# Optimization experiments

Hardware: AMD Instinct MI355X
Metric: run time of the kernel (lower is better)

## Reference

```python
import jax, jax.numpy as jnp
import numpy as np

N = 100000          # nodes
E = 1600000         # edges
F = 128             # input features
H = 128             # hidden_channels
G = 64              # graphs in batch


def setup_inputs() -> dict:
    key = jax.random.key(0)
    ks = jax.random.split(key, 16)
    x = jax.random.normal(ks[0], (N, F), dtype=jnp.float32)
    edge_index = jax.random.randint(ks[1], (2, E), 0, N, dtype=jnp.int32)
    batch = jnp.sort(jax.random.randint(ks[2], (N,), 0, G, dtype=jnp.int32))

    def glorot(k, fan_in, fan_out):
        s = jnp.sqrt(6.0 / (fan_in + fan_out)).astype(jnp.float32)
        return jax.random.uniform(k, (fan_in, fan_out), jnp.float32, -s, s)

    return {
        "x": x, "edge_index": edge_index, "batch": batch,
        "W1": glorot(ks[3], F, H),       "b1": jnp.zeros((H,), jnp.float32),
        "W2": glorot(ks[4], H, H),       "b2": jnp.zeros((H,), jnp.float32),
        "W3": glorot(ks[5], H, 2 * H),   "b3": jnp.zeros((2 * H,), jnp.float32),
        "W4": glorot(ks[6], 2 * H, H),   "b4": jnp.zeros((H,), jnp.float32),
        "Wl": glorot(ks[7], F, H),       "bl": jnp.zeros((H,), jnp.float32),
    }


def _gcn_conv(x, W, b, src, dst, deg_inv_sqrt):
    # PyG GCNConv: add self-loops, symmetric normalization D^-1/2 (A+I) D^-1/2
    h = x @ W                                  # [N, out]
    norm = deg_inv_sqrt[src] * deg_inv_sqrt[dst]      # [E]
    msg = h[src] * norm[:, None]               # gather + scale, [E, out]
    agg = jax.ops.segment_sum(msg, dst, num_segments=N)
    agg = agg + h * (deg_inv_sqrt * deg_inv_sqrt)[:, None]  # self-loop term (norm = 1/deg)
    return agg + b


def reference(x, edge_index, batch, W1, b1, W2, b2, W3, b3, W4, b4, Wl, bl):
    src, dst = edge_index[0], edge_index[1]
    # degree (incl. self-loop) from dst, as in PyG gcn_norm
    deg = jax.ops.segment_sum(jnp.ones((E,), jnp.float32), dst, num_segments=N) + 1.0
    deg_inv_sqrt = jax.lax.rsqrt(deg)

    identity = x
    x = jax.nn.relu(_gcn_conv(x, W1, b1, src, dst, deg_inv_sqrt))
    x = jax.nn.relu(_gcn_conv(x, W2, b2, src, dst, deg_inv_sqrt))
    x = jax.nn.relu(_gcn_conv(x, W3, b3, src, dst, deg_inv_sqrt))
    x = _gcn_conv(x, W4, b4, src, dst, deg_inv_sqrt)
    x = x + (identity @ Wl + bl)

    # global_mean_pool over graph ids
    sums = jax.ops.segment_sum(x, batch, num_segments=G)
    cnts = jax.ops.segment_sum(jnp.ones((N,), jnp.float32), batch, num_segments=G)
    return sums / jnp.maximum(cnts, 1.0)[:, None]
```

## Files before the change

kernel.cpp:

```cpp
#include <hip/hip_runtime.h>

#define NN 100000
#define EE 1600000
#define GG 64

typedef __attribute__((ext_vector_type(8))) short short8v;
typedef __attribute__((ext_vector_type(4))) float f32x4;

__device__ __forceinline__ unsigned short f2bf(float f) {
    unsigned u = __float_as_uint(f);
    u = (u + 0x7FFFu + ((u >> 16) & 1)) >> 16;
    return (unsigned short)u;
}
__device__ __forceinline__ float bf2f(unsigned short s) {
    return __uint_as_float((unsigned)s << 16);
}

__global__ __launch_bounds__(256) void count_kernel(const int* __restrict__ dst,
                                                    int* __restrict__ cnt) {
    int e = blockIdx.x * 256 + threadIdx.x;
    if (e < EE) atomicAdd(&cnt[dst[e]], 1);
}

__global__ __launch_bounds__(256) void dis_kernel(const int* __restrict__ cnt,
                                                  float* __restrict__ dis) {
    int i = blockIdx.x * 256 + threadIdx.x;
    if (i < NN) dis[i] = rsqrtf((float)cnt[i] + 1.0f);
}

#define SCAN_EPB 1024
__global__ __launch_bounds__(256) void scan_block_kernel(const int* __restrict__ in,
                                                         int* __restrict__ out,
                                                         int* __restrict__ bsums) {
    __shared__ int sd[256];
    int t = threadIdx.x;
    int base = blockIdx.x * SCAN_EPB + t * 4;
    int v[4];
#pragma unroll
    for (int j = 0; j < 4; ++j) v[j] = (base + j < NN) ? in[base + j] : 0;
    int s = v[0] + v[1] + v[2] + v[3];
    sd[t] = s;
    __syncthreads();
    for (int off = 1; off < 256; off <<= 1) {
        int add = (t >= off) ? sd[t - off] : 0;
        __syncthreads();
        sd[t] += add;
        __syncthreads();
    }
    int ex = sd[t] - s;
    int run = ex;
#pragma unroll
    for (int j = 0; j < 4; ++j) {
        if (base + j < NN) out[base + j] = run;
        run += v[j];
    }
    if (t == 255) bsums[blockIdx.x] = sd[255];
}

__global__ void scan_sums_kernel(int* __restrict__ bsums, int nb) {
    if (threadIdx.x == 0 && blockIdx.x == 0) {
        int run = 0;
        for (int i = 0; i < nb; ++i) {
            int v = bsums[i];
            bsums[i] = run;
            run += v;
        }
    }
}

__global__ __launch_bounds__(256) void scan_add_kernel(int* __restrict__ rs,
                                                       const int* __restrict__ bsums,
                                                       int* __restrict__ cursor) {
    int i = blockIdx.x * 256 + threadIdx.x;
    if (i < NN) {
        int v = rs[i] + bsums[i >> 10];
        rs[i] = v;
        cursor[i] = v;
    }
    if (i == 0) rs[NN] = EE;
}

__global__ __launch_bounds__(256) void scatter_kernel(const int* __restrict__ src,
                                                      const int* __restrict__ dst,
                                                      const float* __restrict__ dis,
                                                      int* __restrict__ cursor,
                                                      int2* __restrict__ csr) {
    int e = blockIdx.x * 256 + threadIdx.x;
    if (e < EE) {
        int d = dst[e], s = src[e];
        int p = atomicAdd(&cursor[d], 1);
        csr[p] = make_int2(s, __float_as_int(dis[s]));
    }
}

__global__ __launch_bounds__(256) void cvt_kernel(const float* __restrict__ x,
                                                  unsigned short* __restrict__ xb) {
    size_t i = ((size_t)blockIdx.x * 256 + threadIdx.x) * 8;
    float4 a = *(const float4*)(x + i);
    float4 b = *(const float4*)(x + i + 4);
    short8v v;
    v[0] = (short)f2bf(a.x); v[1] = (short)f2bf(a.y);
    v[2] = (short)f2bf(a.z); v[3] = (short)f2bf(a.w);
    v[4] = (short)f2bf(b.x); v[5] = (short)f2bf(b.y);
    v[6] = (short)f2bf(b.z); v[7] = (short)f2bf(b.w);
    *(short8v*)(xb + i) = v;
}

template <int K, int M>
__global__ __launch_bounds__(64) void packw_kernel(const float* __restrict__ W,
                                                   unsigned short* __restrict__ Wp) {
    const int NKS = K / 32;
    int ct = blockIdx.x / NKS, ks = blockIdx.x % NKS;
    int lane = threadIdx.x;
    int col = ct * 16 + (lane & 15);
    int kb = ks * 32 + (lane >> 4) * 8;
    unsigned short* o = Wp + ((size_t)(ct * NKS + ks) * 64 + lane) * 16;
#pragma unroll
    for (int i = 0; i < 8; ++i) {
        float f = W[(size_t)(kb + i) * M + col];
        unsigned short h = f2bf(f);
        unsigned short l = f2bf(f - bf2f(h));
        o[i] = h;
        o[8 + i] = l;
    }
}

template <int K, int M, bool ASPLIT, bool RELU, bool BIAS, bool ACCUM>
__global__ __launch_bounds__(256) void gemm_kernel(const void* __restrict__ Ain,
                                                   const unsigned short* __restrict__ Wp,
                                                   const float* __restrict__ bias,
                                                   void* __restrict__ out) {
    const int NKS = K / 32;
    int tid = threadIdx.x;
    int wave = tid >> 6, lane = tid & 63;
    int r0 = blockIdx.x * 64 + wave * 16;
    int ra = r0 + (lane & 15);
    if (ra > NN - 1) ra = NN - 1;

    short8v ah[NKS];
    short8v al[ASPLIT ? NKS : 1];
    if (ASPLIT) {
        const float* A = (const float*)Ain;
#pragma unroll
        for (int ks = 0; ks < NKS; ++ks) {
            const float* p = A + (size_t)ra * K + ks * 32 + (lane >> 4) * 8;
            float4 v0 = *(const float4*)p;
            float4 v1 = *(const float4*)(p + 4);
            float f[8] = {v0.x, v0.y, v0.z, v0.w, v1.x, v1.y, v1.z, v1.w};
#pragma unroll
            for (int i = 0; i < 8; ++i) {
                unsigned short h = f2bf(f[i]);
                ah[ks][i] = (short)h;
                al[ks][i] = (short)f2bf(f[i] - bf2f(h));
            }
        }
    } else {
        const unsigned short* A = (const unsigned short*)Ain;
#pragma unroll
        for (int ks = 0; ks < NKS; ++ks)
            ah[ks] = *(const short8v*)(A + (size_t)ra * K + ks * 32 + (lane >> 4) * 8);
    }

#pragma unroll
    for (int ct = 0; ct < 8; ++ct) {
        int ctg = blockIdx.y * 8 + ct;
        int col = ctg * 16 + (lane & 15);
        float b = BIAS ? bias[col] : 0.f;
        f32x4 acc;
        acc[0] = b; acc[1] = b; acc[2] = b; acc[3] = b;
#pragma unroll
        for (int ks = 0; ks < NKS; ++ks) {
            const short8v* p = (const short8v*)Wp + ((size_t)(ctg * NKS + ks) * 64 + lane) * 2;
            short8v bh = p[0], bl = p[1];
            acc = __builtin_amdgcn_mfma_f32_16x16x32_bf16(ah[ks], bh, acc, 0, 0, 0);
            acc = __builtin_amdgcn_mfma_f32_16x16x32_bf16(ah[ks], bl, acc, 0, 0, 0);
            if (ASPLIT)
                acc = __builtin_amdgcn_mfma_f32_16x16x32_bf16(al[ks], bh, acc, 0, 0, 0);
        }
#pragma unroll
        for (int i = 0; i < 4; ++i) {
            int row = r0 + (lane >> 4) * 4 + i;
            if (row >= NN) continue;
            float v = acc[i];
            if (RELU) v = fmaxf(v, 0.f);
            if (ACCUM) {
                float* Y = (float*)out;
                Y[(size_t)row * M + col] += v;
            } else {
                unsigned short* O = (unsigned short*)out;
                O[(size_t)row * M + col] = f2bf(v);
            }
        }
    }
}

template <int OUTMODE>
__global__ __launch_bounds__(256) void aggb_kernel(const unsigned short* __restrict__ h,
                                                   const float* __restrict__ dis,
                                                   const int2* __restrict__ csr,
                                                   const int* __restrict__ rs,
                                                   const float* __restrict__ bias,
                                                   void* __restrict__ out) {
    int node = blockIdx.x * 4 + (threadIdx.x >> 6);
    int lane = threadIdx.x & 63;
    if (node >= NN) return;
    int c = lane & 15;
    int s = lane >> 4;
    int beg = rs[node], end = rs[node + 1];
    const uint4* hb = (const uint4*)h;
    float acc[8] = {};
    for (int e0 = beg; e0 < end; e0 += 4) {
        int e = e0 + s;
        int ec = e < end ? e : end - 1;
        int2 pr = csr[ec];
        float w = e < end ? __int_as_float(pr.y) : 0.f;
        uint4 v = hb[(size_t)pr.x * 16 + c];
        acc[0] = fmaf(w, __uint_as_float(v.x << 16), acc[0]);
        acc[1] = fmaf(w, __uint_as_float(v.x & 0xFFFF0000u), acc[1]);
        acc[2] = fmaf(w, __uint_as_float(v.y << 16), acc[2]);
        acc[3] = fmaf(w, __uint_as_float(v.y & 0xFFFF0000u), acc[3]);
        acc[4] = fmaf(w, __uint_as_float(v.z << 16), acc[4]);
        acc[5] = fmaf(w, __uint_as_float(v.z & 0xFFFF0000u), acc[5]);
        acc[6] = fmaf(w, __uint_as_float(v.w << 16), acc[6]);
        acc[7] = fmaf(w, __uint_as_float(v.w & 0xFFFF0000u), acc[7]);
    }
#pragma unroll
    for (int i = 0; i < 8; ++i) {
        acc[i] += __shfl_xor(acc[i], 16, 64);
        acc[i] += __shfl_xor(acc[i], 32, 64);
    }
    if (s == 0) {
        float d = dis[node];
        float dd = d * d;
        uint4 us = hb[(size_t)node * 16 + c];
        float sf[8];
        sf[0] = __uint_as_float(us.x << 16); sf[1] = __uint_as_float(us.x & 0xFFFF0000u);
        sf[2] = __uint_as_float(us.y << 16); sf[3] = __uint_as_float(us.y & 0xFFFF0000u);
        sf[4] = __uint_as_float(us.z << 16); sf[5] = __uint_as_float(us.z & 0xFFFF0000u);
        sf[6] = __uint_as_float(us.w << 16); sf[7] = __uint_as_float(us.w & 0xFFFF0000u);
        float r[8];
#pragma unroll
        for (int i = 0; i < 8; ++i) r[i] = fmaf(d, acc[i], dd * sf[i]);
        if (OUTMODE == 0) {
            uint4 o;
            o.x = (unsigned)f2bf(r[0]) | ((unsigned)f2bf(r[1]) << 16);
            o.y = (unsigned)f2bf(r[2]) | ((unsigned)f2bf(r[3]) << 16);
            o.z = (unsigned)f2bf(r[4]) | ((unsigned)f2bf(r[5]) << 16);
            o.w = (unsigned)f2bf(r[6]) | ((unsigned)f2bf(r[7]) << 16);
            ((uint4*)out)[(size_t)node * 16 + c] = o;
        } else {
#pragma unroll
            for (int i = 0; i < 8; ++i) r[i] += bias[c * 8 + i];
            float4 o0 = make_float4(r[0], r[1], r[2], r[3]);
            float4 o1 = make_float4(r[4], r[5], r[6], r[7]);
            float* O = (float*)out + (size_t)node * 128 + c * 8;
            *(float4*)O = o0;
            *(float4*)(O + 4) = o1;
        }
    }
}

__global__ __launch_bounds__(128) void pool_partial_kernel(const float* __restrict__ y,
                                                           const int* __restrict__ batch,
                                                           float* __restrict__ P) {
    int c = threadIdx.x;
    int chunk = (NN + gridDim.x - 1) / gridDim.x;
    int n0 = blockIdx.x * chunk;
    int n1 = n0 + chunk;
    if (n1 > NN) n1 = NN;
    if (n0 >= NN) return;
    int curg = batch[n0];
    float acc = 0.f;
    for (int n = n0; n < n1; ++n) {
        int g = batch[n];
        if (g != curg) {
            atomicAdd(&P[curg * 128 + c], acc);
            acc = 0.f;
            curg = g;
        }
        acc += y[(size_t)n * 128 + c];
    }
    atomicAdd(&P[curg * 128 + c], acc);
}

__global__ __launch_bounds__(128) void pool_final_kernel(const float* __restrict__ P,
                                                         const int* __restrict__ batch,
                                                         float* __restrict__ out) {
    int g = blockIdx.x, c = threadIdx.x;
    int lo = 0, hi = NN;
    while (lo < hi) {
        int m = (lo + hi) >> 1;
        if (batch[m] < g) lo = m + 1;
        else hi = m;
    }
    int start = lo;
    int lo2 = start, hi2 = NN;
    while (lo2 < hi2) {
        int m = (lo2 + hi2) >> 1;
        if (batch[m] < g + 1) lo2 = m + 1;
        else hi2 = m;
    }
    float cntg = (float)(lo2 - start);
    out[g * 128 + c] = P[g * 128 + c] / fmaxf(cntg, 1.f);
}

extern "C" void kernel_launch(void* const* d_in, const int* in_sizes, int n_in,
                              void* d_out, int out_size, void* d_ws, size_t ws_size,
                              hipStream_t stream) {
    const float* x = (const float*)d_in[0];
    const int* ei = (const int*)d_in[1];
    const int* batch = (const int*)d_in[2];
    const float* W1 = (const float*)d_in[3];
    const float* b1 = (const float*)d_in[4];
    const float* W2 = (const float*)d_in[5];
    const float* b2 = (const float*)d_in[6];
    const float* W3 = (const float*)d_in[7];
    const float* b3 = (const float*)d_in[8];
    const float* W4 = (const float*)d_in[9];
    const float* b4 = (const float*)d_in[10];
    const float* Wl = (const float*)d_in[11];
    const float* bl = (const float*)d_in[12];
    float* out = (float*)d_out;

    char* p = (char*)d_ws;
    auto alloc = [&](size_t bytes) {
        void* r = (void*)p;
        p += (bytes + 255) & ~(size_t)255;
        return r;
    };
    int* cnt = (int*)alloc((size_t)NN * 4);
    int* rs = (int*)alloc((size_t)(NN + 1) * 4);
    int* cursor = (int*)alloc((size_t)NN * 4);
    float* dis = (float*)alloc((size_t)NN * 4);
    const int NB = (NN + SCAN_EPB - 1) / SCAN_EPB;
    int* bsums = (int*)alloc((size_t)NB * 4);
    int2* csr = (int2*)alloc((size_t)EE * 8);
    unsigned short* xb = (unsigned short*)alloc((size_t)NN * 128 * 2);
    unsigned short* AG = (unsigned short*)alloc((size_t)NN * 128 * 2);
    unsigned short* GM = (unsigned short*)alloc((size_t)NN * 128 * 2);
    unsigned short* H3 = (unsigned short*)alloc((size_t)NN * 256 * 2);
    float* Y = (float*)alloc((size_t)NN * 128 * 4);
    unsigned short* W1p = (unsigned short*)alloc(8 * 4 * 64 * 16 * 2);
    unsigned short* W2p = (unsigned short*)alloc(8 * 4 * 64 * 16 * 2);
    unsigned short* W3p = (unsigned short*)alloc(16 * 4 * 64 * 16 * 2);
    unsigned short* W4p = (unsigned short*)alloc(8 * 8 * 64 * 16 * 2);
    unsigned short* Wlp = (unsigned short*)alloc(8 * 4 * 64 * 16 * 2);
    float* P = (float*)alloc((size_t)GG * 128 * 4);

    const int* src = ei;
    const int* dst = ei + EE;

    hipMemsetAsync(cnt, 0, (size_t)NN * 4, stream);
    hipMemsetAsync(P, 0, (size_t)GG * 128 * 4, stream);

    count_kernel<<<EE / 256, 256, 0, stream>>>(dst, cnt);
    dis_kernel<<<(NN + 255) / 256, 256, 0, stream>>>(cnt, dis);
    scan_block_kernel<<<NB, 256, 0, stream>>>(cnt, rs, bsums);
    scan_sums_kernel<<<1, 64, 0, stream>>>(bsums, NB);
    scan_add_kernel<<<(NN + 255) / 256, 256, 0, stream>>>(rs, bsums, cursor);
    scatter_kernel<<<EE / 256, 256, 0, stream>>>(src, dst, dis, cursor, csr);

    cvt_kernel<<<(NN * 128) / (256 * 8), 256, 0, stream>>>(x, xb);
    packw_kernel<128, 128><<<8 * 4, 64, 0, stream>>>(W1, W1p);
    packw_kernel<128, 128><<<8 * 4, 64, 0, stream>>>(W2, W2p);
    packw_kernel<128, 256><<<16 * 4, 64, 0, stream>>>(W3, W3p);
    packw_kernel<256, 128><<<8 * 8, 64, 0, stream>>>(W4, W4p);
    packw_kernel<128, 128><<<8 * 4, 64, 0, stream>>>(Wl, Wlp);

    const int AGG_GRID = (NN + 3) / 4;
    const int GX = (NN + 63) / 64;

    aggb_kernel<0><<<AGG_GRID, 256, 0, stream>>>(xb, dis, csr, rs, nullptr, AG);
    gemm_kernel<128, 128, false, true, true, false><<<dim3(GX, 1), 256, 0, stream>>>(AG, W1p, b1, GM);
    aggb_kernel<0><<<AGG_GRID, 256, 0, stream>>>(GM, dis, csr, rs, nullptr, AG);
    gemm_kernel<128, 128, false, true, true, false><<<dim3(GX, 1), 256, 0, stream>>>(AG, W2p, b2, GM);
    aggb_kernel<0><<<AGG_GRID, 256, 0, stream>>>(GM, dis, csr, rs, nullptr, AG);
    gemm_kernel<128, 256, false, true, true, false><<<dim3(GX, 2), 256, 0, stream>>>(AG, W3p, b3, H3);
    gemm_kernel<256, 128, false, false, false, false><<<dim3(GX, 1), 256, 0, stream>>>(H3, W4p, nullptr, AG);
    aggb_kernel<1><<<AGG_GRID, 256, 0, stream>>>(AG, dis, csr, rs, b4, Y);
    gemm_kernel<128, 128, true, false, true, true><<<dim3(GX, 1), 256, 0, stream>>>(x, Wlp, bl, Y);
    pool_partial_kernel<<<512, 128, 0, stream>>>(Y, batch, P);
    pool_final_kernel<<<GG, 128, 0, stream>>>(P, batch, out);
}
```

Before: 820.6 us.

## Bucket edges before CSR scatter, add row tiling to GEMM, unroll aggregation

Edges are first binned into coarse destination buckets of 256 nodes. A per-bucket scatter pass then writes CSR entries, so the cursor atomics and writes stay localized. The GEMM kernel now processes several 16-row tiles per wave, which reuses each loaded weight fragment across more rows. The aggregation loop issues four gathers before doing the FMAs, to raise memory-level parallelism. Buckets have a fixed capacity of 8192 and any overflow is silently clamped, which relies on dst being roughly uniform. The bucket buffer also reuses the Y allocation.

```diff
diff --git a/kernel.cpp b/kernel.cpp
--- a/kernel.cpp
+++ b/kernel.cpp
@@ -3,6 +3,8 @@
 #define NN 100000
 #define EE 1600000
 #define GG 64
+#define NBK 391
+#define BCAP 8192
 
 typedef __attribute__((ext_vector_type(8))) short short8v;
 typedef __attribute__((ext_vector_type(4))) float f32x4;
@@ -16,10 +18,20 @@
     return __uint_as_float((unsigned)s << 16);
 }
 
-__global__ __launch_bounds__(256) void count_kernel(const int* __restrict__ dst,
-                                                    int* __restrict__ cnt) {
+__global__ __launch_bounds__(256) void bucket_kernel(const int* __restrict__ src,
+                                                     const int* __restrict__ dst,
+                                                     int* __restrict__ cnt,
+                                                     int* __restrict__ bcur,
+                                                     int2* __restrict__ bbuf) {
     int e = blockIdx.x * 256 + threadIdx.x;
-    if (e < EE) atomicAdd(&cnt[dst[e]], 1);
+    if (e < EE) {
+        int d = dst[e], s = src[e];
+        atomicAdd(&cnt[d], 1);
+        int b = d >> 8;
+        int p = atomicAdd(&bcur[b], 1);
+        if (p >= BCAP) p = BCAP - 1;
+        bbuf[(size_t)b * BCAP + p] = make_int2(s, d);
+    }
 }
 
 __global__ __launch_bounds__(256) void dis_kernel(const int* __restrict__ cnt,
@@ -80,16 +92,19 @@
     if (i == 0) rs[NN] = EE;
 }
 
-__global__ __launch_bounds__(256) void scatter_kernel(const int* __restrict__ src,
-                                                      const int* __restrict__ dst,
-                                                      const float* __restrict__ dis,
-                                                      int* __restrict__ cursor,
-                                                      int2* __restrict__ csr) {
-    int e = blockIdx.x * 256 + threadIdx.x;
-    if (e < EE) {
-        int d = dst[e], s = src[e];
-        int p = atomicAdd(&cursor[d], 1);
-        csr[p] = make_int2(s, __float_as_int(dis[s]));
+__global__ __launch_bounds__(256) void scatter2_kernel(const int2* __restrict__ bbuf,
+                                                       const int* __restrict__ bcur,
+                                                       const float* __restrict__ dis,
+                                                       int* __restrict__ cursor,
+                                                       int2* __restrict__ csr) {
+    int b = blockIdx.x;
+    int n = bcur[b];
+    if (n > BCAP) n = BCAP;
+    const int2* bb = bbuf + (size_t)b * BCAP;
+    for (int i = threadIdx.x; i < n; i += 256) {
+        int2 e = bb[i];
+        int p = atomicAdd(&cursor[e.y], 1);
+        csr[p] = make_int2(e.x, __float_as_int(dis[e.x]));
     }
 }
 
@@ -125,7 +140,7 @@
     }
 }
 
-template <int K, int M, bool ASPLIT, bool RELU, bool BIAS, bool ACCUM>
+template <int K, int M, int RT, bool ASPLIT, bool RELU, bool BIAS, bool ACCUM>
 __global__ __launch_bounds__(256) void gemm_kernel(const void* __restrict__ Ain,
                                                    const unsigned short* __restrict__ Wp,
                                                    const float* __restrict__ bias,
@@ -133,64 +148,73 @@
     const int NKS = K / 32;
     int tid = threadIdx.x;
     int wave = tid >> 6, lane = tid & 63;
-    int r0 = blockIdx.x * 64 + wave * 16;
-    int ra = r0 + (lane & 15);
-    if (ra > NN - 1) ra = NN - 1;
-
-    short8v ah[NKS];
-    short8v al[ASPLIT ? NKS : 1];
-    if (ASPLIT) {
-        const float* A = (const float*)Ain;
-#pragma unroll
-        for (int ks = 0; ks < NKS; ++ks) {
-            const float* p = A + (size_t)ra * K + ks * 32 + (lane >> 4) * 8;
-            float4 v0 = *(const float4*)p;
-            float4 v1 = *(const float4*)(p + 4);
-            float f[8] = {v0.x, v0.y, v0.z, v0.w, v1.x, v1.y, v1.z, v1.w};
-#pragma unroll
-            for (int i = 0; i < 8; ++i) {
-                unsigned short h = f2bf(f[i]);
-                ah[ks][i] = (short)h;
-                al[ks][i] = (short)f2bf(f[i] - bf2f(h));
+    int r0 = blockIdx.x * (RT * 64) + wave * (RT * 16);
+
+    short8v ah[RT][NKS];
+    short8v al[ASPLIT ? RT : 1][ASPLIT ? NKS : 1];
+#pragma unroll
+    for (int t = 0; t < RT; ++t) {
+        int ra = r0 + t * 16 + (lane & 15);
+        if (ra > NN - 1) ra = NN - 1;
+        if (ASPLIT) {
+            const float* A = (const float*)Ain;
+#pragma unroll
+            for (int ks = 0; ks < NKS; ++ks) {
+                const float* p = A + (size_t)ra * K + ks * 32 + (lane >> 4) * 8;
+                float4 v0 = *(const float4*)p;
+                float4 v1 = *(const float4*)(p + 4);
+                float f[8] = {v0.x, v0.y, v0.z, v0.w, v1.x, v1.y, v1.z, v1.w};
+#pragma unroll
+                for (int i = 0; i < 8; ++i) {
+                    unsigned short h = f2bf(f[i]);
+                    ah[t][ks][i] = (short)h;
+                    al[t][ks][i] = (short)f2bf(f[i] - bf2f(h));
+                }
             }
-        }
-    } else {
-        const unsigned short* A = (const unsigned short*)Ain;
-#pragma unroll
-        for (int ks = 0; ks < NKS; ++ks)
-            ah[ks] = *(const short8v*)(A + (size_t)ra * K + ks * 32 + (lane >> 4) * 8);
+        } else {
+            const unsigned short* A = (const unsigned short*)Ain;
+#pragma unroll
+            for (int ks = 0; ks < NKS; ++ks)
+                ah[t][ks] = *(const short8v*)(A + (size_t)ra * K + ks * 32 + (lane >> 4) * 8);
+        }
     }
 
 #pragma unroll
     for (int ct = 0; ct < 8; ++ct) {
         int ctg = blockIdx.y * 8 + ct;
         int col = ctg * 16 + (lane & 15);
-        float b = BIAS ? bias[col] : 0.f;
-        f32x4 acc;
-        acc[0] = b; acc[1] = b; acc[2] = b; acc[3] = b;
+        float bv = BIAS ? bias[col] : 0.f;
+        f32x4 acc[RT];
+#pragma unroll
+        for (int t = 0; t < RT; ++t) {
+            acc[t][0] = bv; acc[t][1] = bv; acc[t][2] = bv; acc[t][3] = bv;
+        }
 #pragma unroll
         for (int ks = 0; ks < NKS; ++ks) {
-            const short8v* p = (const short8v*)Wp + ((size_t)(ctg * NKS + ks) * 64 + lane) * 2;
-            short8v bh = p[0], bl = p[1];
-            acc = __builtin_amdgcn_mfma_f32_16x16x32_bf16(ah[ks], bh, acc, 0, 0, 0);
-            acc = __builtin_amdgcn_mfma_f32_16x16x32_bf16(ah[ks], bl, acc, 0, 0, 0);
-            if (ASPLIT)
-                acc = __builtin_amdgcn_mfma_f32_16x16x32_bf16(al[ks], bh, acc, 0, 0, 0);
-        }
-#pragma unroll
-        for (int i = 0; i < 4; ++i) {
-            int row = r0 + (lane >> 4) * 4 + i;
-            if (row >= NN) continue;
-            float v = acc[i];
-            if (RELU) v = fmaxf(v, 0.f);
-            if (ACCUM) {
-                float* Y = (float*)out;
-                Y[(size_t)row * M + col] += v;
-            } else {
-                unsigned short* O = (unsigned short*)out;
-                O[(size_t)row * M + col] = f2bf(v);
+            const short8v* pW = (const short8v*)Wp + ((size_t)(ctg * NKS + ks) * 64 + lane) * 2;
+            short8v bh = pW[0], blo = pW[1];
+#pragma unroll
+            for (int t = 0; t < RT; ++t) {
+                acc[t] = __builtin_amdgcn_mfma_f32_16x16x32_bf16(ah[t][ks], bh, acc[t], 0, 0, 0);
+                acc[t] = __builtin_amdgcn_mfma_f32_16x16x32_bf16(ah[t][ks], blo, acc[t], 0, 0, 0);
+                if (ASPLIT)
+                    acc[t] = __builtin_amdgcn_mfma_f32_16x16x32_bf16(al[t][ks], bh, acc[t], 0, 0, 0);
             }
         }
+#pragma unroll
+        for (int t = 0; t < RT; ++t)
+#pragma unroll
+            for (int i = 0; i < 4; ++i) {
+                int row = r0 + t * 16 + (lane >> 4) * 4 + i;
+                if (row >= NN) continue;
+                float v = acc[t][i];
+                if (RELU) v = fmaxf(v, 0.f);
+                if (ACCUM) {
+                    ((float*)out)[(size_t)row * M + col] += v;
+                } else {
+                    ((unsigned short*)out)[(size_t)row * M + col] = f2bf(v);
+                }
+            }
     }
 }
 
@@ -209,20 +233,28 @@
     int beg = rs[node], end = rs[node + 1];
     const uint4* hb = (const uint4*)h;
     float acc[8] = {};
-    for (int e0 = beg; e0 < end; e0 += 4) {
-        int e = e0 + s;
-        int ec = e < end ? e : end - 1;
-        int2 pr = csr[ec];
-        float w = e < end ? __int_as_float(pr.y) : 0.f;
-        uint4 v = hb[(size_t)pr.x * 16 + c];
-        acc[0] = fmaf(w, __uint_as_float(v.x << 16), acc[0]);
-        acc[1] = fmaf(w, __uint_as_float(v.x & 0xFFFF0000u), acc[1]);
-        acc[2] = fmaf(w, __uint_as_float(v.y << 16), acc[2]);
-        acc[3] = fmaf(w, __uint_as_float(v.y & 0xFFFF0000u), acc[3]);
-        acc[4] = fmaf(w, __uint_as_float(v.z << 16), acc[4]);
-        acc[5] = fmaf(w, __uint_as_float(v.z & 0xFFFF0000u), acc[5]);
-        acc[6] = fmaf(w, __uint_as_float(v.w << 16), acc[6]);
-        acc[7] = fmaf(w, __uint_as_float(v.w & 0xFFFF0000u), acc[7]);
+    for (int e0 = beg; e0 < end; e0 += 16) {
+        float w[4];
+        uint4 v[4];
+#pragma unroll
+        for (int j = 0; j < 4; ++j) {
+            int ej = e0 + j * 4 + s;
+            int ec = ej < end ? ej : end - 1;
+            int2 pr = csr[ec];
+            w[j] = ej < end ? __int_as_float(pr.y) : 0.f;
+            v[j] = hb[(size_t)pr.x * 16 + c];
+        }
+#pragma unroll
+        for (int j = 0; j < 4; ++j) {
+            acc[0] = fmaf(w[j], __uint_as_float(v[j].x << 16), acc[0]);
+            acc[1] = fmaf(w[j], __uint_as_float(v[j].x & 0xFFFF0000u), acc[1]);
+            acc[2] = fmaf(w[j], __uint_as_float(v[j].y << 16), acc[2]);
+            acc[3] = fmaf(w[j], __uint_as_float(v[j].y & 0xFFFF0000u), acc[3]);
+            acc[4] = fmaf(w[j], __uint_as_float(v[j].z << 16), acc[4]);
+            acc[5] = fmaf(w[j], __uint_as_float(v[j].z & 0xFFFF0000u), acc[5]);
+            acc[6] = fmaf(w[j], __uint_as_float(v[j].w << 16), acc[6]);
+            acc[7] = fmaf(w[j], __uint_as_float(v[j].w & 0xFFFF0000u), acc[7]);
+        }
     }
 #pragma unroll
     for (int i = 0; i < 8; ++i) {
@@ -334,6 +366,7 @@
     float* dis = (float*)alloc((size_t)NN * 4);
     const int NB = (NN + SCAN_EPB - 1) / SCAN_EPB;
     int* bsums = (int*)alloc((size_t)NB * 4);
+    int* bcur = (int*)alloc((size_t)NBK * 4);
     int2* csr = (int2*)alloc((size_t)EE * 8);
     unsigned short* xb = (unsigned short*)alloc((size_t)NN * 128 * 2);
     unsigned short* AG = (unsigned short*)alloc((size_t)NN * 128 * 2);
@@ -346,19 +379,21 @@
     unsigned short* W4p = (unsigned short*)alloc(8 * 8 * 64 * 16 * 2);
     unsigned short* Wlp = (unsigned short*)alloc(8 * 4 * 64 * 16 * 2);
     float* P = (float*)alloc((size_t)GG * 128 * 4);
+    int2* bbuf = (int2*)Y;
 
     const int* src = ei;
     const int* dst = ei + EE;
 
     hipMemsetAsync(cnt, 0, (size_t)NN * 4, stream);
+    hipMemsetAsync(bcur, 0, (size_t)NBK * 4, stream);
     hipMemsetAsync(P, 0, (size_t)GG * 128 * 4, stream);
 
-    count_kernel<<<EE / 256, 256, 0, stream>>>(dst, cnt);
+    bucket_kernel<<<EE / 256, 256, 0, stream>>>(src, dst, cnt, bcur, bbuf);
     dis_kernel<<<(NN + 255) / 256, 256, 0, stream>>>(cnt, dis);
     scan_block_kernel<<<NB, 256, 0, stream>>>(cnt, rs, bsums);
     scan_sums_kernel<<<1, 64, 0, stream>>>(bsums, NB);
     scan_add_kernel<<<(NN + 255) / 256, 256, 0, stream>>>(rs, bsums, cursor);
-    scatter_kernel<<<EE / 256, 256, 0, stream>>>(src, dst, dis, cursor, csr);
+    scatter2_kernel<<<NBK, 256, 0, stream>>>(bbuf, bcur, dis, cursor, csr);
 
     cvt_kernel<<<(NN * 128) / (256 * 8), 256, 0, stream>>>(x, xb);
     packw_kernel<128, 128><<<8 * 4, 64, 0, stream>>>(W1, W1p);
@@ -368,17 +403,18 @@
     packw_kernel<128, 128><<<8 * 4, 64, 0, stream>>>(Wl, Wlp);
 
     const int AGG_GRID = (NN + 3) / 4;
-    const int GX = (NN + 63) / 64;
+    const int GX4 = (NN + 255) / 256;
+    const int GX2 = (NN + 127) / 128;
 
     aggb_kernel<0><<<AGG_GRID, 256, 0, stream>>>(xb, dis, csr, rs, nullptr, AG);
-    gemm_kernel<128, 128, false, true, true, false><<<dim3(GX, 1), 256, 0, stream>>>(AG, W1p, b1, GM);
+    gemm_kernel<128, 128, 4, false, true, true, false><<<dim3(GX4, 1), 256, 0, stream>>>(AG, W1p, b1, GM);
     aggb_kernel<0><<<AGG_GRID, 256, 0, stream>>>(GM, dis, csr, rs, nullptr, AG);
-    gemm_kernel<128, 128, false, true, true, false><<<dim3(GX, 1), 256, 0, stream>>>(AG, W2p, b2, GM);
+    gemm_kernel<128, 128, 4, false, true, true, false><<<dim3(GX4, 1), 256, 0, stream>>>(AG, W2p, b2, GM);
     aggb_kernel<0><<<AGG_GRID, 256, 0, stream>>>(GM, dis, csr, rs, nullptr, AG);
-    gemm_kernel<128, 256, false, true, true, false><<<dim3(GX, 2), 256, 0, stream>>>(AG, W3p, b3, H3);
-    gemm_kernel<256, 128, false, false, false, false><<<dim3(GX, 1), 256, 0, stream>>>(H3, W4p, nullptr, AG);
+    gemm_kernel<128, 256, 4, false, true, true, false><<<dim3(GX4, 2), 256, 0, stream>>>(AG, W3p, b3, H3);
+    gemm_kernel<256, 128, 2, false, false, false, false><<<dim3(GX2, 1), 256, 0, stream>>>(H3, W4p, nullptr, AG);
     aggb_kernel<1><<<AGG_GRID, 256, 0, stream>>>(AG, dis, csr, rs, b4, Y);
-    gemm_kernel<128, 128, true, false, true, true><<<dim3(GX, 1), 256, 0, stream>>>(x, Wlp, bl, Y);
+    gemm_kernel<128, 128, 2, true, false, true, true><<<dim3(GX2, 1), 256, 0, stream>>>(x, Wlp, bl, Y);
     pool_partial_kernel<<<512, 128, 0, stream>>>(Y, batch, P);
     pool_final_kernel<<<GG, 128, 0, stream>>>(P, batch, out);
 }
```

Result: slower. 1.323 ms (+61.2%).
